# Optimization experiments

Hardware: AMD Instinct MI355X
Metric: run time of the kernel (lower is better)

## Reference

```python
import jax, jax.numpy as jnp
import numpy as np

EPS = 1e-5


def setup_inputs() -> dict:
    key = jax.random.key(0)
    N, L, D, L1, OUT = 64, 2050, 768, 512, 300
    ks = jax.random.split(key, 4)
    t1 = jax.random.normal(ks[0], (N, L, D), dtype=jnp.float32)
    # ragged word/NP spans over the 2048 content tokens (after dropping CLS/SEP)
    rng = np.random.default_rng(0)
    lengths = rng.integers(1, 5, size=(N, L1))          # span lengths 1..4, total <= 2048
    ends = np.cumsum(lengths, axis=1)
    starts = ends - lengths
    n_valid = rng.integers(L1 // 2, L1 + 1, size=N)
    mask = np.arange(L1)[None, :] >= n_valid[:, None]    # True = padded span (masked)
    W_lin_ = jax.random.normal(ks[1], (D, OUT), dtype=jnp.float32) * 0.02
    b_lin_ = jnp.zeros((OUT,), jnp.float32)
    gamma = jnp.ones((OUT,), jnp.float32)
    beta = jnp.zeros((OUT,), jnp.float32)
    W_lin = jax.random.normal(ks[2], (OUT, 1), dtype=jnp.float32) * 0.02
    b_lin = jnp.zeros((1,), jnp.float32)
    return dict(
        t1=t1,
        span_starts=jnp.asarray(starts, jnp.int32),
        span_ends=jnp.asarray(ends, jnp.int32),
        key_padding_mask=jnp.asarray(mask),
        W_lin_=W_lin_, b_lin_=b_lin_, gamma=gamma, beta=beta,
        W_lin=W_lin, b_lin=b_lin, lam=1,
    )


def reference(t1, span_starts, span_ends, key_padding_mask,
              W_lin_, b_lin_, gamma, beta, W_lin, b_lin, lam):
    tok = t1[:, 1:-1, :]                                   # (N, Ltok, D) drop CLS/SEP
    # segment mean over contiguous ragged spans via inclusive prefix sums
    cs = jnp.concatenate([jnp.zeros_like(tok[:, :1]), jnp.cumsum(tok, axis=1)], axis=1)  # (N, Ltok+1, D)
    gather = lambda idx: jnp.take_along_axis(cs, idx[:, :, None], axis=1)
    counts = (span_ends - span_starts).astype(tok.dtype)[..., None]
    pooled = (gather(span_ends) - gather(span_starts)) / counts  # (N, L1, D)
    # linear projection D -> OUT, then LayerNorm over last dim
    x = pooled @ W_lin_ + b_lin_                           # (N, L1, OUT)
    mu = jnp.mean(x, axis=-1, keepdims=True)
    var = jnp.mean((x - mu) ** 2, axis=-1, keepdims=True)
    x = (x - mu) * jax.lax.rsqrt(var + EPS) * gamma + beta
    # importance score: linear -> masked softmax over spans, expanded to OUT
    score = (x @ W_lin + b_lin)[..., 0]                    # (N, L1)
    score = jnp.where(key_padding_mask, -jnp.inf, score)
    p = jax.nn.softmax(score * lam, axis=1)
    score_out = jnp.broadcast_to(p[..., None], x.shape)    # (N, L1, OUT)
    return x, score_out
```

## Files before the change

### kernel.cpp

```cpp
#include <hip/hip_runtime.h>
#include <math.h>

#define NB    64
#define LSEQ  2050
#define DIN   768
#define NSPAN 512
#define DOUT  300
#define MROWS (NB * NSPAN)
#define EPSV  1e-5f

#define BM    128
#define BK    32
#define NF_W  5

typedef __bf16 bf16x8 __attribute__((ext_vector_type(8)));
typedef __bf16 bf16x4 __attribute__((ext_vector_type(4)));
typedef float  f32x4  __attribute__((ext_vector_type(4)));

#define GLOAD16(gp, lp) \
  __builtin_amdgcn_global_load_lds((const __attribute__((address_space(1))) void*)(gp), \
                                   (__attribute__((address_space(3))) void*)(lp), 16, 0, 0)

__device__ __forceinline__ float scalar_to_f(const void* p) {
    unsigned bits = *(const unsigned*)p;
    if (bits < 0x00800000u) return (float)(int)bits;
    return __uint_as_float(bits);
}

__device__ __forceinline__ float wred_sum(float x) {
    #pragma unroll
    for (int off = 32; off > 0; off >>= 1) x += __shfl_xor(x, off);
    return x;
}

__global__ __launch_bounds__(192) void pool_kernel(
    const float* __restrict__ t1, const int* __restrict__ starts,
    const int* __restrict__ ends, __bf16* __restrict__ Ahi, __bf16* __restrict__ Alo)
{
    int r = blockIdx.x;
    int b = r >> 9;
    int s0 = starts[r], e0 = ends[r];
    float inv = 1.0f / (float)(e0 - s0);
    int d = threadIdx.x * 4;
    const float* base = t1 + ((size_t)b * LSEQ + 1) * DIN + d;
    float4 acc = make_float4(0.f, 0.f, 0.f, 0.f);
    for (int t = s0; t < e0; ++t) {
        float4 v = *(const float4*)(base + (size_t)t * DIN);
        acc.x += v.x; acc.y += v.y; acc.z += v.z; acc.w += v.w;
    }
    acc.x *= inv; acc.y *= inv; acc.z *= inv; acc.w *= inv;
    __bf16 h0 = (__bf16)acc.x, h1 = (__bf16)acc.y, h2 = (__bf16)acc.z, h3 = (__bf16)acc.w;
    __bf16 l0 = (__bf16)(acc.x - (float)h0);
    __bf16 l1 = (__bf16)(acc.y - (float)h1);
    __bf16 l2 = (__bf16)(acc.z - (float)h2);
    __bf16 l3 = (__bf16)(acc.w - (float)h3);
    size_t o = (size_t)r * DIN + d;
    bf16x4 hv = {h0, h1, h2, h3};
    bf16x4 lv = {l0, l1, l2, l3};
    *(bf16x4*)(Ahi + o) = hv;
    *(bf16x4*)(Alo + o) = lv;
}

__global__ __launch_bounds__(256) void wsplit_kernel(
    const float* __restrict__ W, __bf16* __restrict__ Wthi, __bf16* __restrict__ Wtlo)
{
    int idx = blockIdx.x * 256 + threadIdx.x;
    int c = idx / DIN, k = idx % DIN;
    float v = (c < DOUT) ? W[(size_t)k * DOUT + c] : 0.f;
    __bf16 h = (__bf16)v;
    Wthi[idx] = h;
    Wtlo[idx] = (__bf16)(v - (float)h);
}

__global__ __launch_bounds__(256) void maskflag_kernel(
    const unsigned* __restrict__ mw, int* __restrict__ flag)
{
    __shared__ int any;
    if (threadIdx.x == 0) any = 0;
    __syncthreads();
    int loc = 0;
    for (int i = threadIdx.x; i < 8192; i += 256)
        loc |= (mw[i] > 1u) ? 1 : 0;
    if (loc) atomicOr(&any, 1);
    __syncthreads();
    if (threadIdx.x == 0) *flag = any;
}

__global__ __launch_bounds__(512) void gemm_ln_kernel(
    const __bf16* __restrict__ Ahi, const __bf16* __restrict__ Alo,
    const __bf16* __restrict__ Wthi, const __bf16* __restrict__ Wtlo,
    const float* __restrict__ bias, const float* __restrict__ gamma,
    const float* __restrict__ beta, const float* __restrict__ W2,
    const float* __restrict__ b2, float* __restrict__ X, float* __restrict__ score)
{
    __shared__ __align__(16) char smem[32768 + 81920 + 4096 + 1024];
    char*  Abuf = smem;
    char*  Bbuf = smem + 32768;
    float* red  = (float*)(smem + 32768 + 81920);
    float* murs = red + 1024;

    const int tid  = threadIdx.x;
    const int lane = tid & 63;
    const int wv   = tid >> 6;
    const int wm   = wv >> 2;
    const int wn   = wv & 3;
    const int row0 = blockIdx.x * BM;
    const int l15  = lane & 15;
    const int kc   = lane >> 4;

    f32x4 acc[4][NF_W];
    #pragma unroll
    for (int mf = 0; mf < 4; ++mf)
        #pragma unroll
        for (int i = 0; i < NF_W; ++i)
            acc[mf][i] = (f32x4){0.f, 0.f, 0.f, 0.f};

    int asw[4], bsw[NF_W];
    #pragma unroll
    for (int mf = 0; mf < 4; ++mf) {
        int a = (wm * 64 + mf * 16 + l15) * 64 + (kc << 4);
        asw[mf] = a ^ (((a >> 7) & 3) << 4);
    }
    #pragma unroll
    for (int i = 0; i < NF_W; ++i) {
        int c = (wn * NF_W + i) * 16 + l15;
        int a = c * 64 + (kc << 4);
        bsw[i] = a ^ (((a >> 7) & 3) << 4);
    }

    const int aRow  = tid >> 2;
    const int aCsw  = (tid & 3) ^ ((tid >> 3) & 3);
    const int wbase = (tid >> 6) << 10;

    #define STAGE(buf, k0)                                                          \
    do {                                                                            \
        _Pragma("unroll")                                                           \
        for (int pl = 0; pl < 2; ++pl) {                                            \
            const __bf16* sA = pl ? Alo : Ahi;                                      \
            const char* gA = (const char*)(sA + (size_t)(row0 + aRow) * DIN + (k0)) \
                             + (aCsw << 4);                                         \
            GLOAD16(gA, Abuf + ((buf) * 2 + pl) * 8192 + wbase);                    \
        }                                                                           \
        _Pragma("unroll")                                                           \
        for (int pl = 0; pl < 2; ++pl) {                                            \
            const __bf16* sB = pl ? Wtlo : Wthi;                                    \
            _Pragma("unroll")                                                       \
            for (int j = 0; j < 3; ++j) {                                           \
                int o = j * 8192 + tid * 16;                                        \
                if (o < 20480) {                                                    \
                    int c   = o >> 6;                                               \
                    int csw = ((o >> 4) & 3) ^ ((o >> 7) & 3);                      \
                    const char* gB = (const char*)(sB + (size_t)c * DIN + (k0))     \
                                     + (csw << 4);                                  \
                    GLOAD16(gB, Bbuf + ((buf) * 2 + pl) * 20480 + (o & ~1023));     \
                }                                                                   \
            }                                                                       \
        }                                                                           \
    } while (0)

    STAGE(0, 0);
    asm volatile("s_waitcnt vmcnt(0)" ::: "memory");
    __syncthreads();

    int cur = 0;
    for (int t = 0; t < DIN / BK; ++t) {
        if (t < DIN / BK - 1) STAGE(cur ^ 1, (t + 1) * BK);

        bf16x8 bh[NF_W], bl[NF_W];
        #pragma unroll
        for (int i = 0; i < NF_W; ++i) {
            bh[i] = *(const bf16x8*)(Bbuf + (cur * 2 + 0) * 20480 + bsw[i]);
            bl[i] = *(const bf16x8*)(Bbuf + (cur * 2 + 1) * 20480 + bsw[i]);
        }
        #pragma unroll
        for (int mf = 0; mf < 4; ++mf) {
            bf16x8 ah = *(const bf16x8*)(Abuf + (cur * 2 + 0) * 8192 + asw[mf]);
            bf16x8 al = *(const bf16x8*)(Abuf + (cur * 2 + 1) * 8192 + asw[mf]);
            #pragma unroll
            for (int i = 0; i < NF_W; ++i) {
                acc[mf][i] = __builtin_amdgcn_mfma_f32_16x16x32_bf16(ah, bh[i], acc[mf][i], 0, 0, 0);
                acc[mf][i] = __builtin_amdgcn_mfma_f32_16x16x32_bf16(ah, bl[i], acc[mf][i], 0, 0, 0);
                acc[mf][i] = __builtin_amdgcn_mfma_f32_16x16x32_bf16(al, bh[i], acc[mf][i], 0, 0, 0);
            }
        }
        asm volatile("s_waitcnt vmcnt(0)" ::: "memory");
        __syncthreads();
        cur ^= 1;
    }

    int   cc[NF_W];
    float gv[NF_W], bv[NF_W], wv2[NF_W];
    #pragma unroll
    for (int i = 0; i < NF_W; ++i) {
        int c = (wn * NF_W + i) * 16 + l15;
        cc[i] = c;
        bool ok = c < DOUT;
        float bb = ok ? bias[c] : 0.f;
        gv[i]  = ok ? gamma[c] : 0.f;
        bv[i]  = ok ? beta[c]  : 0.f;
        wv2[i] = ok ? W2[c]    : 0.f;
        #pragma unroll
        for (int mf = 0; mf < 4; ++mf) {
            acc[mf][i].x += bb; acc[mf][i].y += bb;
            acc[mf][i].z += bb; acc[mf][i].w += bb;
        }
    }

    #pragma unroll
    for (int mf = 0; mf < 4; ++mf) {
        #pragma unroll
        for (int r = 0; r < 4; ++r) {
            float s = 0.f, q = 0.f;
            #pragma unroll
            for (int i = 0; i < NF_W; ++i) {
                float v = (r == 0) ? acc[mf][i].x : (r == 1) ? acc[mf][i].y
                         : (r == 2) ? acc[mf][i].z : acc[mf][i].w;
                s += v; q = fmaf(v, v, q);
            }
            #pragma unroll
            for (int off = 1; off < 16; off <<= 1) {
                s += __shfl_xor(s, off);
                q += __shfl_xor(q, off);
            }
            if (l15 == 0) {
                int row = wm * 64 + mf * 16 + kc * 4 + r;
                red[(wn * 128 + row) * 2 + 0] = s;
                red[(wn * 128 + row) * 2 + 1] = q;
            }
        }
    }
    __syncthreads();
    if (tid < 128) {
        float s = red[tid*2] + red[(128+tid)*2] + red[(256+tid)*2] + red[(384+tid)*2];
        float q = red[tid*2+1] + red[(128+tid)*2+1] + red[(256+tid)*2+1] + red[(384+tid)*2+1];
        float mu = s * (1.0f / DOUT);
        float var = q * (1.0f / DOUT) - mu * mu;
        murs[tid*2]   = mu;
        murs[tid*2+1] = rsqrtf(var + EPSV);
    }
    __syncthreads();

    #pragma unroll
    for (int mf = 0; mf < 4; ++mf) {
        #pragma unroll
        for (int r = 0; r < 4; ++r) {
            int row = wm * 64 + mf * 16 + kc * 4 + r;
            float mu = murs[row*2], rs = murs[row*2+1];
            float sc = 0.f;
            #pragma unroll
            for (int i = 0; i < NF_W; ++i) {
                float v = (r == 0) ? acc[mf][i].x : (r == 1) ? acc[mf][i].y
                         : (r == 2) ? acc[mf][i].z : acc[mf][i].w;
                float xn = (v - mu) * rs * gv[i] + bv[i];
                if (cc[i] < DOUT)
                    X[(size_t)(row0 + row) * DOUT + cc[i]] = xn;
                sc = fmaf(xn, wv2[i], sc);
            }
            #pragma unroll
            for (int off = 1; off < 16; off <<= 1) sc += __shfl_xor(sc, off);
            if (l15 == 0) red[(wn * 128 + row) * 2] = sc;
        }
    }
    __syncthreads();
    if (tid < 128) {
        float sc = red[tid*2] + red[(128+tid)*2] + red[(256+tid)*2] + red[(384+tid)*2];
        score[row0 + tid] = sc + b2[0];
    }
}

__global__ __launch_bounds__(512) void softmax_kernel(
    const float* __restrict__ score, const void* __restrict__ maskp,
    const int* __restrict__ flag, const void* __restrict__ lamp,
    float* __restrict__ p)
{
    __shared__ float redm[8], reds[8];
    int b = blockIdx.x, t = threadIdx.x;
    int i = (b << 9) + t;
    bool masked = (*flag) ? (((const unsigned char*)maskp)[i] != 0)
                          : (((const int*)maskp)[i] != 0);
    float lam = scalar_to_f(lamp);
    float s = masked ? -INFINITY : score[i] * lam;

    float m = s;
    #pragma unroll
    for (int off = 32; off > 0; off >>= 1) m = fmaxf(m, __shfl_xor(m, off));
    if ((t & 63) == 0) redm[t >> 6] = m;
    __syncthreads();
    m = redm[0];
    #pragma unroll
    for (int w = 1; w < 8; ++w) m = fmaxf(m, redm[w]);

    float e = masked ? 0.f : expf(s - m);
    float su = wred_sum(e);
    if ((t & 63) == 0) reds[t >> 6] = su;
    __syncthreads();
    su = reds[0];
    #pragma unroll
    for (int w = 1; w < 8; ++w) su += reds[w];

    p[i] = e / su;
}

__global__ __launch_bounds__(256) void bcast_kernel(
    const float* __restrict__ p, float* __restrict__ out2)
{
    const int total = MROWS * (DOUT / 4);
    int stride = gridDim.x * blockDim.x;
    for (int idx = blockIdx.x * blockDim.x + threadIdx.x; idx < total; idx += stride) {
        int row = idx / 75;
        float pv = p[row];
        ((float4*)out2)[idx] = make_float4(pv, pv, pv, pv);
    }
}

extern "C" void kernel_launch(void* const* d_in, const int* in_sizes, int n_in,
                              void* d_out, int out_size, void* d_ws, size_t ws_size,
                              hipStream_t stream)
{
    const float* t1     = (const float*)d_in[0];
    const int*   starts = (const int*)d_in[1];
    const int*   ends   = (const int*)d_in[2];
    const void*  mask   = d_in[3];
    const float* Wlin   = (const float*)d_in[4];
    const float* blin   = (const float*)d_in[5];
    const float* gamma  = (const float*)d_in[6];
    const float* beta   = (const float*)d_in[7];
    const float* W2     = (const float*)d_in[8];
    const float* b2     = (const float*)d_in[9];
    const void*  lam    = d_in[10];

    float* x_out = (float*)d_out;
    float* out2  = x_out + (size_t)MROWS * DOUT;

    __bf16* Ahi  = (__bf16*)d_ws;
    __bf16* Alo  = Ahi + (size_t)MROWS * DIN;
    __bf16* Wthi = Alo + (size_t)MROWS * DIN;
    __bf16* Wtlo = Wthi + 320 * DIN;
    float*  score = (float*)(Wtlo + 320 * DIN);
    float*  p     = score + MROWS;
    int*    flag  = (int*)(p + MROWS);

    hipLaunchKernelGGL(pool_kernel,     dim3(MROWS), dim3(192), 0, stream, t1, starts, ends, Ahi, Alo);
    hipLaunchKernelGGL(wsplit_kernel,   dim3(960),   dim3(256), 0, stream, Wlin, Wthi, Wtlo);
    hipLaunchKernelGGL(maskflag_kernel, dim3(1),     dim3(256), 0, stream, (const unsigned*)mask, flag);
    hipLaunchKernelGGL(gemm_ln_kernel,  dim3(MROWS / BM), dim3(512), 0, stream,
                       Ahi, Alo, Wthi, Wtlo, blin, gamma, beta, W2, b2, x_out, score);
    hipLaunchKernelGGL(softmax_kernel,  dim3(NB),    dim3(512), 0, stream, score, mask, flag, lam, p);
    hipLaunchKernelGGL(bcast_kernel,    dim3(2048),  dim3(256), 0, stream, p, out2);
}
```

Before: 612.9 us.

## Fuse span pooling into GEMM-LayerNorm kernel and read weights directly from global

Removes the separate pooling kernel and its bf16 hi/lo intermediate buffers. The GEMM kernel now gathers up to four span tokens per row from t1, averages and splits them into LDS, and prefetches the next K slice in registers. The block tile shrinks to 64 rows with 256 threads, and B fragments are loaded straight from global memory instead of being staged in LDS. The intent is to avoid writing and re-reading a large intermediate. The cost is uncoalesced B loads and gather latency inside the GEMM loop, and the unrolled gather assumes spans are at most four tokens long. The broadcast kernel is also rewritten to give each thread a contiguous chunk of a row.

```diff
diff --git a/kernel.cpp b/kernel.cpp
--- a/kernel.cpp
+++ b/kernel.cpp
@@ -9,17 +9,12 @@
 #define MROWS (NB * NSPAN)
 #define EPSV  1e-5f
 
-#define BM    128
+#define BM    64
 #define BK    32
 #define NF_W  5
 
 typedef __bf16 bf16x8 __attribute__((ext_vector_type(8)));
-typedef __bf16 bf16x4 __attribute__((ext_vector_type(4)));
 typedef float  f32x4  __attribute__((ext_vector_type(4)));
-
-#define GLOAD16(gp, lp) \
-  __builtin_amdgcn_global_load_lds((const __attribute__((address_space(1))) void*)(gp), \
-                                   (__attribute__((address_space(3))) void*)(lp), 16, 0, 0)
 
 __device__ __forceinline__ float scalar_to_f(const void* p) {
     unsigned bits = *(const unsigned*)p;
@@ -33,33 +28,7 @@
     return x;
 }
 
-__global__ __launch_bounds__(192) void pool_kernel(
-    const float* __restrict__ t1, const int* __restrict__ starts,
-    const int* __restrict__ ends, __bf16* __restrict__ Ahi, __bf16* __restrict__ Alo)
-{
-    int r = blockIdx.x;
-    int b = r >> 9;
-    int s0 = starts[r], e0 = ends[r];
-    float inv = 1.0f / (float)(e0 - s0);
-    int d = threadIdx.x * 4;
-    const float* base = t1 + ((size_t)b * LSEQ + 1) * DIN + d;
-    float4 acc = make_float4(0.f, 0.f, 0.f, 0.f);
-    for (int t = s0; t < e0; ++t) {
-        float4 v = *(const float4*)(base + (size_t)t * DIN);
-        acc.x += v.x; acc.y += v.y; acc.z += v.z; acc.w += v.w;
-    }
-    acc.x *= inv; acc.y *= inv; acc.z *= inv; acc.w *= inv;
-    __bf16 h0 = (__bf16)acc.x, h1 = (__bf16)acc.y, h2 = (__bf16)acc.z, h3 = (__bf16)acc.w;
-    __bf16 l0 = (__bf16)(acc.x - (float)h0);
-    __bf16 l1 = (__bf16)(acc.y - (float)h1);
-    __bf16 l2 = (__bf16)(acc.z - (float)h2);
-    __bf16 l3 = (__bf16)(acc.w - (float)h3);
-    size_t o = (size_t)r * DIN + d;
-    bf16x4 hv = {h0, h1, h2, h3};
-    bf16x4 lv = {l0, l1, l2, l3};
-    *(bf16x4*)(Ahi + o) = hv;
-    *(bf16x4*)(Alo + o) = lv;
-}
+__device__ __forceinline__ int sw(int a) { return a ^ (((a >> 7) & 3) << 4); }
 
 __global__ __launch_bounds__(256) void wsplit_kernel(
     const float* __restrict__ W, __bf16* __restrict__ Wthi, __bf16* __restrict__ Wtlo)
@@ -86,27 +55,50 @@
     if (threadIdx.x == 0) *flag = any;
 }
 
-__global__ __launch_bounds__(512) void gemm_ln_kernel(
-    const __bf16* __restrict__ Ahi, const __bf16* __restrict__ Alo,
+__global__ __launch_bounds__(256, 2) void fused_kernel(
+    const float* __restrict__ t1, const int* __restrict__ starts,
+    const int* __restrict__ ends,
     const __bf16* __restrict__ Wthi, const __bf16* __restrict__ Wtlo,
     const float* __restrict__ bias, const float* __restrict__ gamma,
     const float* __restrict__ beta, const float* __restrict__ W2,
     const float* __restrict__ b2, float* __restrict__ X, float* __restrict__ score)
 {
-    __shared__ __align__(16) char smem[32768 + 81920 + 4096 + 1024];
-    char*  Abuf = smem;
-    char*  Bbuf = smem + 32768;
-    float* red  = (float*)(smem + 32768 + 81920);
-    float* murs = red + 1024;
+    __shared__ __align__(16) char Abuf[16384];
+    __shared__ float red[512];
+    __shared__ float murs[128];
 
     const int tid  = threadIdx.x;
     const int lane = tid & 63;
-    const int wv   = tid >> 6;
-    const int wm   = wv >> 2;
-    const int wn   = wv & 3;
-    const int row0 = blockIdx.x * BM;
+    const int wn   = tid >> 6;
     const int l15  = lane & 15;
     const int kc   = lane >> 4;
+    const int row0 = blockIdx.x * BM;
+    const int b    = row0 >> 9;
+
+    const int pr = tid >> 2;
+    const int kq = tid & 3;
+    const int grow = row0 + pr;
+    const int s0 = starts[grow], e0 = ends[grow];
+    const float inv = 1.0f / (float)(e0 - s0);
+    const float* tokbase = t1 + ((size_t)b * LSEQ + 1) * DIN + kq * 8;
+    const size_t o0 = (size_t)s0 * DIN;
+    const size_t o1 = (size_t)((s0 + 1 < e0) ? s0 + 1 : e0 - 1) * DIN;
+    const size_t o2 = (size_t)((s0 + 2 < e0) ? s0 + 2 : e0 - 1) * DIN;
+    const size_t o3 = (size_t)((s0 + 3 < e0) ? s0 + 3 : e0 - 1) * DIN;
+    const float m1 = (s0 + 1 < e0) ? 1.f : 0.f;
+    const float m2 = (s0 + 2 < e0) ? 1.f : 0.f;
+    const float m3 = (s0 + 3 < e0) ? 1.f : 0.f;
+
+    const int wsw = sw(pr * 64 + kq * 16);
+
+    int asw_[4];
+    #pragma unroll
+    for (int mf = 0; mf < 4; ++mf)
+        asw_[mf] = sw((mf * 16 + l15) * 64 + kc * 16);
+
+    int ci[NF_W];
+    #pragma unroll
+    for (int i = 0; i < NF_W; ++i) ci[i] = (wn * NF_W + i) * 16 + l15;
 
     f32x4 acc[4][NF_W];
     #pragma unroll
@@ -115,67 +107,55 @@
         for (int i = 0; i < NF_W; ++i)
             acc[mf][i] = (f32x4){0.f, 0.f, 0.f, 0.f};
 
-    int asw[4], bsw[NF_W];
-    #pragma unroll
-    for (int mf = 0; mf < 4; ++mf) {
-        int a = (wm * 64 + mf * 16 + l15) * 64 + (kc << 4);
-        asw[mf] = a ^ (((a >> 7) & 3) << 4);
-    }
-    #pragma unroll
-    for (int i = 0; i < NF_W; ++i) {
-        int c = (wn * NF_W + i) * 16 + l15;
-        int a = c * 64 + (kc << 4);
-        bsw[i] = a ^ (((a >> 7) & 3) << 4);
-    }
-
-    const int aRow  = tid >> 2;
-    const int aCsw  = (tid & 3) ^ ((tid >> 3) & 3);
-    const int wbase = (tid >> 6) << 10;
-
-    #define STAGE(buf, k0)                                                          \
-    do {                                                                            \
-        _Pragma("unroll")                                                           \
-        for (int pl = 0; pl < 2; ++pl) {                                            \
-            const __bf16* sA = pl ? Alo : Ahi;                                      \
-            const char* gA = (const char*)(sA + (size_t)(row0 + aRow) * DIN + (k0)) \
-                             + (aCsw << 4);                                         \
-            GLOAD16(gA, Abuf + ((buf) * 2 + pl) * 8192 + wbase);                    \
-        }                                                                           \
-        _Pragma("unroll")                                                           \
-        for (int pl = 0; pl < 2; ++pl) {                                            \
-            const __bf16* sB = pl ? Wtlo : Wthi;                                    \
-            _Pragma("unroll")                                                       \
-            for (int j = 0; j < 3; ++j) {                                           \
-                int o = j * 8192 + tid * 16;                                        \
-                if (o < 20480) {                                                    \
-                    int c   = o >> 6;                                               \
-                    int csw = ((o >> 4) & 3) ^ ((o >> 7) & 3);                      \
-                    const char* gB = (const char*)(sB + (size_t)c * DIN + (k0))     \
-                                     + (csw << 4);                                  \
-                    GLOAD16(gB, Bbuf + ((buf) * 2 + pl) * 20480 + (o & ~1023));     \
-                }                                                                   \
-            }                                                                       \
-        }                                                                           \
+    float4 pA0, pA1, pB0, pB1, pC0, pC1, pD0, pD1;
+    #define AISSUE(k0)                                              \
+    do {                                                            \
+        const float* tb = tokbase + (k0);                           \
+        pA0 = *(const float4*)(tb + o0); pA1 = *(const float4*)(tb + o0 + 4); \
+        pB0 = *(const float4*)(tb + o1); pB1 = *(const float4*)(tb + o1 + 4); \
+        pC0 = *(const float4*)(tb + o2); pC1 = *(const float4*)(tb + o2 + 4); \
+        pD0 = *(const float4*)(tb + o3); pD1 = *(const float4*)(tb + o3 + 4); \
     } while (0)
 
-    STAGE(0, 0);
-    asm volatile("s_waitcnt vmcnt(0)" ::: "memory");
-    __syncthreads();
-
-    int cur = 0;
+    AISSUE(0);
+
     for (int t = 0; t < DIN / BK; ++t) {
-        if (t < DIN / BK - 1) STAGE(cur ^ 1, (t + 1) * BK);
+        const int k0 = t * BK;
+        const int bbase = (t & 1) * 8192;
+
+        float v0 = (pA0.x + m1 * pB0.x + m2 * pC0.x + m3 * pD0.x) * inv;
+        float v1 = (pA0.y + m1 * pB0.y + m2 * pC0.y + m3 * pD0.y) * inv;
+        float v2 = (pA0.z + m1 * pB0.z + m2 * pC0.z + m3 * pD0.z) * inv;
+        float v3 = (pA0.w + m1 * pB0.w + m2 * pC0.w + m3 * pD0.w) * inv;
+        float v4 = (pA1.x + m1 * pB1.x + m2 * pC1.x + m3 * pD1.x) * inv;
+        float v5 = (pA1.y + m1 * pB1.y + m2 * pC1.y + m3 * pD1.y) * inv;
+        float v6 = (pA1.z + m1 * pB1.z + m2 * pC1.z + m3 * pD1.z) * inv;
+        float v7 = (pA1.w + m1 * pB1.w + m2 * pC1.w + m3 * pD1.w) * inv;
+        __bf16 h0 = (__bf16)v0, h1 = (__bf16)v1, h2 = (__bf16)v2, h3 = (__bf16)v3;
+        __bf16 h4 = (__bf16)v4, h5 = (__bf16)v5, h6 = (__bf16)v6, h7 = (__bf16)v7;
+        bf16x8 hv = {h0, h1, h2, h3, h4, h5, h6, h7};
+        bf16x8 lv = {(__bf16)(v0 - (float)h0), (__bf16)(v1 - (float)h1),
+                     (__bf16)(v2 - (float)h2), (__bf16)(v3 - (float)h3),
+                     (__bf16)(v4 - (float)h4), (__bf16)(v5 - (float)h5),
+                     (__bf16)(v6 - (float)h6), (__bf16)(v7 - (float)h7)};
+        *(bf16x8*)(Abuf + bbase + wsw)        = hv;
+        *(bf16x8*)(Abuf + bbase + 4096 + wsw) = lv;
+
+        if (t < DIN / BK - 1) AISSUE(k0 + BK);
+
+        __syncthreads();
 
         bf16x8 bh[NF_W], bl[NF_W];
         #pragma unroll
         for (int i = 0; i < NF_W; ++i) {
-            bh[i] = *(const bf16x8*)(Bbuf + (cur * 2 + 0) * 20480 + bsw[i]);
-            bl[i] = *(const bf16x8*)(Bbuf + (cur * 2 + 1) * 20480 + bsw[i]);
+            size_t off = (size_t)ci[i] * DIN + k0 + kc * 8;
+            bh[i] = *(const bf16x8*)(Wthi + off);
+            bl[i] = *(const bf16x8*)(Wtlo + off);
         }
         #pragma unroll
         for (int mf = 0; mf < 4; ++mf) {
-            bf16x8 ah = *(const bf16x8*)(Abuf + (cur * 2 + 0) * 8192 + asw[mf]);
-            bf16x8 al = *(const bf16x8*)(Abuf + (cur * 2 + 1) * 8192 + asw[mf]);
+            bf16x8 ah = *(const bf16x8*)(Abuf + bbase + asw_[mf]);
+            bf16x8 al = *(const bf16x8*)(Abuf + bbase + 4096 + asw_[mf]);
             #pragma unroll
             for (int i = 0; i < NF_W; ++i) {
                 acc[mf][i] = __builtin_amdgcn_mfma_f32_16x16x32_bf16(ah, bh[i], acc[mf][i], 0, 0, 0);
@@ -183,22 +163,16 @@
                 acc[mf][i] = __builtin_amdgcn_mfma_f32_16x16x32_bf16(al, bh[i], acc[mf][i], 0, 0, 0);
             }
         }
-        asm volatile("s_waitcnt vmcnt(0)" ::: "memory");
-        __syncthreads();
-        cur ^= 1;
-    }
-
-    int   cc[NF_W];
-    float gv[NF_W], bv[NF_W], wv2[NF_W];
+    }
+
+    float gv[NF_W], bvv[NF_W], wv2[NF_W];
     #pragma unroll
     for (int i = 0; i < NF_W; ++i) {
-        int c = (wn * NF_W + i) * 16 + l15;
-        cc[i] = c;
-        bool ok = c < DOUT;
-        float bb = ok ? bias[c] : 0.f;
-        gv[i]  = ok ? gamma[c] : 0.f;
-        bv[i]  = ok ? beta[c]  : 0.f;
-        wv2[i] = ok ? W2[c]    : 0.f;
+        bool ok = ci[i] < DOUT;
+        float bb = ok ? bias[ci[i]] : 0.f;
+        gv[i]  = ok ? gamma[ci[i]] : 0.f;
+        bvv[i] = ok ? beta[ci[i]]  : 0.f;
+        wv2[i] = ok ? W2[ci[i]]    : 0.f;
         #pragma unroll
         for (int mf = 0; mf < 4; ++mf) {
             acc[mf][i].x += bb; acc[mf][i].y += bb;
@@ -209,12 +183,12 @@
     #pragma unroll
     for (int mf = 0; mf < 4; ++mf) {
         #pragma unroll
-        for (int r = 0; r < 4; ++r) {
+        for (int rr = 0; rr < 4; ++rr) {
             float s = 0.f, q = 0.f;
             #pragma unroll
             for (int i = 0; i < NF_W; ++i) {
-                float v = (r == 0) ? acc[mf][i].x : (r == 1) ? acc[mf][i].y
-                         : (r == 2) ? acc[mf][i].z : acc[mf][i].w;
+                float v = (rr == 0) ? acc[mf][i].x : (rr == 1) ? acc[mf][i].y
+                         : (rr == 2) ? acc[mf][i].z : acc[mf][i].w;
                 s += v; q = fmaf(v, v, q);
             }
             #pragma unroll
@@ -223,16 +197,16 @@
                 q += __shfl_xor(q, off);
             }
             if (l15 == 0) {
-                int row = wm * 64 + mf * 16 + kc * 4 + r;
-                red[(wn * 128 + row) * 2 + 0] = s;
-                red[(wn * 128 + row) * 2 + 1] = q;
-            }
-        }
-    }
-    __syncthreads();
-    if (tid < 128) {
-        float s = red[tid*2] + red[(128+tid)*2] + red[(256+tid)*2] + red[(384+tid)*2];
-        float q = red[tid*2+1] + red[(128+tid)*2+1] + red[(256+tid)*2+1] + red[(384+tid)*2+1];
+                int row = mf * 16 + kc * 4 + rr;
+                red[(wn * 64 + row) * 2 + 0] = s;
+                red[(wn * 64 + row) * 2 + 1] = q;
+            }
+        }
+    }
+    __syncthreads();
+    if (tid < 64) {
+        float s = red[tid*2] + red[(64+tid)*2] + red[(128+tid)*2] + red[(192+tid)*2];
+        float q = red[tid*2+1] + red[(64+tid)*2+1] + red[(128+tid)*2+1] + red[(192+tid)*2+1];
         float mu = s * (1.0f / DOUT);
         float var = q * (1.0f / DOUT) - mu * mu;
         murs[tid*2]   = mu;
@@ -243,27 +217,27 @@
     #pragma unroll
     for (int mf = 0; mf < 4; ++mf) {
         #pragma unroll
-        for (int r = 0; r < 4; ++r) {
-            int row = wm * 64 + mf * 16 + kc * 4 + r;
+        for (int rr = 0; rr < 4; ++rr) {
+            int row = mf * 16 + kc * 4 + rr;
             float mu = murs[row*2], rs = murs[row*2+1];
             float sc = 0.f;
             #pragma unroll
             for (int i = 0; i < NF_W; ++i) {
-                float v = (r == 0) ? acc[mf][i].x : (r == 1) ? acc[mf][i].y
-                         : (r == 2) ? acc[mf][i].z : acc[mf][i].w;
-                float xn = (v - mu) * rs * gv[i] + bv[i];
-                if (cc[i] < DOUT)
-                    X[(size_t)(row0 + row) * DOUT + cc[i]] = xn;
+                float v = (rr == 0) ? acc[mf][i].x : (rr == 1) ? acc[mf][i].y
+                         : (rr == 2) ? acc[mf][i].z : acc[mf][i].w;
+                float xn = (v - mu) * rs * gv[i] + bvv[i];
+                if (ci[i] < DOUT)
+                    X[(size_t)(row0 + row) * DOUT + ci[i]] = xn;
                 sc = fmaf(xn, wv2[i], sc);
             }
             #pragma unroll
             for (int off = 1; off < 16; off <<= 1) sc += __shfl_xor(sc, off);
-            if (l15 == 0) red[(wn * 128 + row) * 2] = sc;
-        }
-    }
-    __syncthreads();
-    if (tid < 128) {
-        float sc = red[tid*2] + red[(128+tid)*2] + red[(256+tid)*2] + red[(384+tid)*2];
+            if (l15 == 0) red[(wn * 64 + row) * 2] = sc;
+        }
+    }
+    __syncthreads();
+    if (tid < 64) {
+        float sc = red[tid*2] + red[(64+tid)*2] + red[(128+tid)*2] + red[(192+tid)*2];
         score[row0 + tid] = sc + b2[0];
     }
 }
@@ -304,13 +278,15 @@
 __global__ __launch_bounds__(256) void bcast_kernel(
     const float* __restrict__ p, float* __restrict__ out2)
 {
-    const int total = MROWS * (DOUT / 4);
-    int stride = gridDim.x * blockDim.x;
-    for (int idx = blockIdx.x * blockDim.x + threadIdx.x; idx < total; idx += stride) {
-        int row = idx / 75;
-        float pv = p[row];
-        ((float4*)out2)[idx] = make_float4(pv, pv, pv, pv);
-    }
+    int g = blockIdx.x * 256 + threadIdx.x;
+    int row  = g >> 2;
+    int part = g & 3;
+    float pv = p[row];
+    float4 v = make_float4(pv, pv, pv, pv);
+    float4* dst = (float4*)(out2 + (size_t)row * DOUT);
+    int st = part * 19;
+    int en = (part < 3) ? st + 19 : 75;
+    for (int i = st; i < en; ++i) dst[i] = v;
 }
 
 extern "C" void kernel_launch(void* const* d_in, const int* in_sizes, int n_in,
@@ -332,19 +308,16 @@
     float* x_out = (float*)d_out;
     float* out2  = x_out + (size_t)MROWS * DOUT;
 
-    __bf16* Ahi  = (__bf16*)d_ws;
-    __bf16* Alo  = Ahi + (size_t)MROWS * DIN;
-    __bf16* Wthi = Alo + (size_t)MROWS * DIN;
+    __bf16* Wthi = (__bf16*)d_ws;
     __bf16* Wtlo = Wthi + 320 * DIN;
     float*  score = (float*)(Wtlo + 320 * DIN);
     float*  p     = score + MROWS;
     int*    flag  = (int*)(p + MROWS);
 
-    hipLaunchKernelGGL(pool_kernel,     dim3(MROWS), dim3(192), 0, stream, t1, starts, ends, Ahi, Alo);
-    hipLaunchKernelGGL(wsplit_kernel,   dim3(960),   dim3(256), 0, stream, Wlin, Wthi, Wtlo);
-    hipLaunchKernelGGL(maskflag_kernel, dim3(1),     dim3(256), 0, stream, (const unsigned*)mask, flag);
-    hipLaunchKernelGGL(gemm_ln_kernel,  dim3(MROWS / BM), dim3(512), 0, stream,
-                       Ahi, Alo, Wthi, Wtlo, blin, gamma, beta, W2, b2, x_out, score);
-    hipLaunchKernelGGL(softmax_kernel,  dim3(NB),    dim3(512), 0, stream, score, mask, flag, lam, p);
-    hipLaunchKernelGGL(bcast_kernel,    dim3(2048),  dim3(256), 0, stream, p, out2);
-}
+    hipLaunchKernelGGL(wsplit_kernel,   dim3(960), dim3(256), 0, stream, Wlin, Wthi, Wtlo);
+    hipLaunchKernelGGL(maskflag_kernel, dim3(1),   dim3(256), 0, stream, (const unsigned*)mask, flag);
+    hipLaunchKernelGGL(fused_kernel,    dim3(MROWS / BM), dim3(256), 0, stream,
+                       t1, starts, ends, Wthi, Wtlo, blin, gamma, beta, W2, b2, x_out, score);
+    hipLaunchKernelGGL(softmax_kernel,  dim3(NB),  dim3(512), 0, stream, score, mask, flag, lam, p);
+    hipLaunchKernelGGL(bcast_kernel,    dim3(512), dim3(256), 0, stream, p, out2);
+}
```

New measurement: 595.4 us. 1.03x faster.
